# Performance work log

Measured on AMD Instinct MI355X. Metric: run time of the kernel, lower is better.

Reference implementation:

```python
import jax, jax.numpy as jnp
import numpy as np

ETA_MU = 0.01
ETA_VAR = 0.02
T, D = 32768, 1024


def setup_inputs() -> dict:
    key = jax.random.key(0)
    x = jax.random.normal(key, (T, D), dtype=jnp.float32)
    return {"x": x}


def reference(x):
    # x: [T, D]. Initial state: column mean and (unbiased) std, as in torch.mean/torch.std.
    mu0 = jnp.mean(x, axis=0)
    var0 = jnp.std(x, axis=0, ddof=1)  # torch.std default is unbiased; stored into 'var' slot

    eta_mu = jnp.float32(ETA_MU)
    eta_var = jnp.float32(ETA_VAR)

    def step(carry, xt):
        mu, var = carry
        mu = mu + eta_mu * (xt - mu)                      # in-place mu update (uses new mu below)
        var = var * (1 - eta_var) + eta_var * (xt - mu) ** 2
        norm = (xt - mu) / jnp.sqrt(var)
        return (mu, var), (norm, mu, var)

    _, (norm_x, mus, vars_) = jax.lax.scan(step, (mu0, var0), x)
    additional_info = jnp.concatenate([mus, vars_], axis=-1)  # [T, 2D]
    return norm_x, additional_info
```

## Files before the change

kernel.cpp:

```cpp
#include <hip/hip_runtime.h>
#include <math.h>


#define T_DIM 32768
#define D_DIM 1024
#define CHUNK 128
#define CLEN  (T_DIM / CHUNK)
#define ETA_MU_F 0.01f
#define ETA_VAR_F 0.02f

__global__ __launch_bounds__(256) void k_chunk_summary(
    const float* __restrict__ x, float* __restrict__ ws) {
    const int g = blockIdx.x * 256 + threadIdx.x;
    const int d = g & (D_DIM - 1);
    const int c = g >> 10;
    const float a = 1.0f - ETA_MU_F;
    const float b = 1.0f - ETA_VAR_F;

    float s = 0.0f, s2 = 0.0f;
    float m = 0.0f;
    float q0 = 0.0f, q1 = 0.0f, q2 = 0.0f;
    float p = 1.0f;

    const float* xp = x + (size_t)c * CLEN * D_DIM + d;
#pragma unroll 4
    for (int k = 0; k < CLEN; ++k) {
        float xv = xp[(size_t)k * D_DIM];
        s  += xv;
        s2 += xv * xv;
        m = m + ETA_MU_F * (xv - m);
        p *= a;
        float dv = xv - m;
        q0 = b * q0 + ETA_VAR_F * dv * dv;
        q1 = b * q1 - 2.0f * ETA_VAR_F * dv * p;
        q2 = b * q2 + ETA_VAR_F * p * p;
    }
    const int n = CHUNK * D_DIM;
    ws[0 * n + g] = s;
    ws[1 * n + g] = s2;
    ws[2 * n + g] = m;
    ws[3 * n + g] = q0;
    ws[4 * n + g] = q1;
    ws[5 * n + g] = q2;
}

__global__ __launch_bounds__(256) void k_scan(
    float* __restrict__ ws, float a_pow, float b_pow) {
    const int d = blockIdx.x * 256 + threadIdx.x;
    const int n = CHUNK * D_DIM;
    const float* sum  = ws + 0 * n;
    const float* sum2 = ws + 1 * n;
    const float* bmu  = ws + 2 * n;
    const float* q0   = ws + 3 * n;
    const float* q1   = ws + 4 * n;
    const float* q2   = ws + 5 * n;
    float* mu_in  = ws + 6 * n;
    float* var_in = ws + 7 * n;

    float s = 0.0f, s2 = 0.0f;
#pragma unroll 8
    for (int c = 0; c < CHUNK; ++c) {
        s  += sum[c * D_DIM + d];
        s2 += sum2[c * D_DIM + d];
    }
    float mu0 = s / (float)T_DIM;
    float v0  = (s2 - (float)T_DIM * mu0 * mu0) / (float)(T_DIM - 1);
    float std0 = sqrtf(fmaxf(v0, 0.0f));

    float mu = mu0;
    float var = std0;
#pragma unroll 4
    for (int c = 0; c < CHUNK; ++c) {
        int idx = c * D_DIM + d;
        mu_in[idx]  = mu;
        var_in[idx] = var;
        float mu_next = a_pow * mu + bmu[idx];
        var = b_pow * var + q0[idx] + mu * (q1[idx] + q2[idx] * mu);
        mu = mu_next;
    }
}

__global__ __launch_bounds__(256) void k_replay(
    const float* __restrict__ x, const float* __restrict__ ws,
    float* __restrict__ out) {
    const int g = blockIdx.x * 256 + threadIdx.x;
    const int d = g & (D_DIM - 1);
    const int c = g >> 10;
    const int n = CHUNK * D_DIM;

    float mu  = ws[6 * n + g];
    float var = ws[7 * n + g];

    const size_t t0 = (size_t)c * CLEN;
    const float* xp = x + t0 * D_DIM + d;
    float* norm_out = out + t0 * D_DIM + d;
    float* info = out + (size_t)T_DIM * D_DIM + t0 * (2 * D_DIM) + d;

#pragma unroll 4
    for (int k = 0; k < CLEN; ++k) {
        float xv = xp[(size_t)k * D_DIM];
        mu = mu + ETA_MU_F * (xv - mu);
        float diff = xv - mu;
        var = (1.0f - ETA_VAR_F) * var + ETA_VAR_F * diff * diff;
        norm_out[(size_t)k * D_DIM] = diff / sqrtf(var);
        info[(size_t)k * (2 * D_DIM)]         = mu;
        info[(size_t)k * (2 * D_DIM) + D_DIM] = var;
    }
}

extern "C" void kernel_launch(void* const* d_in, const int* in_sizes, int n_in,
                              void* d_out, int out_size, void* d_ws, size_t ws_size,
                              hipStream_t stream) {
    const float* x = (const float*)d_in[0];
    float* out = (float*)d_out;
    float* ws = (float*)d_ws;

    float a_pow = (float)pow(1.0 - 0.01, (double)CLEN);
    float b_pow = (float)pow(1.0 - 0.02, (double)CLEN);

    const int n = CHUNK * D_DIM;
    hipLaunchKernelGGL(k_chunk_summary, dim3(n / 256), dim3(256), 0, stream, x, ws);
    hipLaunchKernelGGL(k_scan, dim3(D_DIM / 256), dim3(256), 0, stream, ws, a_pow, b_pow);
    hipLaunchKernelGGL(k_replay, dim3(n / 256), dim3(256), 0, stream, x, ws, out);
}
```

Before: 577.7 us.

## Increase chunk count, vectorize float4 passes, fold q2 to host constant, nontemporal stores

Raises the number of time chunks from 128 to 512, which shortens each thread's serial recurrence and gives more parallelism, at the cost of a longer sequential scan over chunks. Chunk-summary and replay kernels now process four columns per thread with float4 loads and stores. The replay writes its outputs with nontemporal stores. The per-chunk q2 term, which depends only on constants, is precomputed on the host as a scalar, removing one workspace array and its loads. The scan kernel uses 64-thread blocks so more blocks spread across CUs, though its serial loop over 512 chunks is now longer.

```diff
diff --git a/kernel.cpp b/kernel.cpp
--- a/kernel.cpp
+++ b/kernel.cpp
@@ -4,58 +4,59 @@
 
 #define T_DIM 32768
 #define D_DIM 1024
-#define CHUNK 128
+#define CHUNK 512
 #define CLEN  (T_DIM / CHUNK)
 #define ETA_MU_F 0.01f
 #define ETA_VAR_F 0.02f
 
+typedef float vf4 __attribute__((ext_vector_type(4)));
+
 __global__ __launch_bounds__(256) void k_chunk_summary(
     const float* __restrict__ x, float* __restrict__ ws) {
-    const int g = blockIdx.x * 256 + threadIdx.x;
-    const int d = g & (D_DIM - 1);
-    const int c = g >> 10;
+    const int c = blockIdx.x;
+    const int j = threadIdx.x;
+    const int n = CHUNK * D_DIM;
     const float a = 1.0f - ETA_MU_F;
     const float b = 1.0f - ETA_VAR_F;
 
-    float s = 0.0f, s2 = 0.0f;
-    float m = 0.0f;
-    float q0 = 0.0f, q1 = 0.0f, q2 = 0.0f;
+    vf4 s  = {0.0f, 0.0f, 0.0f, 0.0f};
+    vf4 s2 = {0.0f, 0.0f, 0.0f, 0.0f};
+    vf4 m  = {0.0f, 0.0f, 0.0f, 0.0f};
+    vf4 q0 = {0.0f, 0.0f, 0.0f, 0.0f};
+    vf4 q1 = {0.0f, 0.0f, 0.0f, 0.0f};
     float p = 1.0f;
 
-    const float* xp = x + (size_t)c * CLEN * D_DIM + d;
-#pragma unroll 4
+    const vf4* xp = (const vf4*)(x + (size_t)c * CLEN * D_DIM) + j;
+#pragma unroll 8
     for (int k = 0; k < CLEN; ++k) {
-        float xv = xp[(size_t)k * D_DIM];
+        vf4 xv = xp[(size_t)k * (D_DIM / 4)];
+        p *= a;
         s  += xv;
         s2 += xv * xv;
-        m = m + ETA_MU_F * (xv - m);
-        p *= a;
-        float dv = xv - m;
-        q0 = b * q0 + ETA_VAR_F * dv * dv;
-        q1 = b * q1 - 2.0f * ETA_VAR_F * dv * p;
-        q2 = b * q2 + ETA_VAR_F * p * p;
+        m  += ETA_MU_F * (xv - m);
+        vf4 dv = xv - m;
+        q0 = b * q0 + ETA_VAR_F * (dv * dv);
+        q1 = b * q1 - (2.0f * ETA_VAR_F * p) * dv;
     }
-    const int n = CHUNK * D_DIM;
-    ws[0 * n + g] = s;
-    ws[1 * n + g] = s2;
-    ws[2 * n + g] = m;
-    ws[3 * n + g] = q0;
-    ws[4 * n + g] = q1;
-    ws[5 * n + g] = q2;
+    const int base = c * D_DIM + 4 * j;
+    *(vf4*)(ws + 0 * n + base) = s;
+    *(vf4*)(ws + 1 * n + base) = s2;
+    *(vf4*)(ws + 2 * n + base) = m;
+    *(vf4*)(ws + 3 * n + base) = q0;
+    *(vf4*)(ws + 4 * n + base) = q1;
 }
 
-__global__ __launch_bounds__(256) void k_scan(
-    float* __restrict__ ws, float a_pow, float b_pow) {
-    const int d = blockIdx.x * 256 + threadIdx.x;
+__global__ __launch_bounds__(64) void k_scan(
+    float* __restrict__ ws, float a_pow, float b_pow, float q2c) {
+    const int d = blockIdx.x * 64 + threadIdx.x;
     const int n = CHUNK * D_DIM;
     const float* sum  = ws + 0 * n;
     const float* sum2 = ws + 1 * n;
     const float* bmu  = ws + 2 * n;
     const float* q0   = ws + 3 * n;
     const float* q1   = ws + 4 * n;
-    const float* q2   = ws + 5 * n;
-    float* mu_in  = ws + 6 * n;
-    float* var_in = ws + 7 * n;
+    float* mu_in  = ws + 5 * n;
+    float* var_in = ws + 6 * n;
 
     float s = 0.0f, s2 = 0.0f;
 #pragma unroll 8
@@ -75,7 +76,7 @@
         mu_in[idx]  = mu;
         var_in[idx] = var;
         float mu_next = a_pow * mu + bmu[idx];
-        var = b_pow * var + q0[idx] + mu * (q1[idx] + q2[idx] * mu);
+        var = b_pow * var + q0[idx] + mu * (q1[idx] + q2c * mu);
         mu = mu_next;
     }
 }
@@ -83,28 +84,35 @@
 __global__ __launch_bounds__(256) void k_replay(
     const float* __restrict__ x, const float* __restrict__ ws,
     float* __restrict__ out) {
-    const int g = blockIdx.x * 256 + threadIdx.x;
-    const int d = g & (D_DIM - 1);
-    const int c = g >> 10;
+    const int c = blockIdx.x;
+    const int j = threadIdx.x;
     const int n = CHUNK * D_DIM;
+    const int base = c * D_DIM + 4 * j;
 
-    float mu  = ws[6 * n + g];
-    float var = ws[7 * n + g];
+    vf4 mu  = *(const vf4*)(ws + 5 * n + base);
+    vf4 var = *(const vf4*)(ws + 6 * n + base);
 
     const size_t t0 = (size_t)c * CLEN;
-    const float* xp = x + t0 * D_DIM + d;
-    float* norm_out = out + t0 * D_DIM + d;
-    float* info = out + (size_t)T_DIM * D_DIM + t0 * (2 * D_DIM) + d;
+    const vf4* xp = (const vf4*)(x + t0 * D_DIM) + j;
+    vf4* norm_out = (vf4*)(out + t0 * D_DIM) + j;
+    float* info_base = out + (size_t)T_DIM * D_DIM + t0 * (2 * D_DIM);
+    vf4* mu_out  = (vf4*)(info_base) + j;
+    vf4* var_out = (vf4*)(info_base + D_DIM) + j;
 
 #pragma unroll 4
     for (int k = 0; k < CLEN; ++k) {
-        float xv = xp[(size_t)k * D_DIM];
-        mu = mu + ETA_MU_F * (xv - mu);
-        float diff = xv - mu;
-        var = (1.0f - ETA_VAR_F) * var + ETA_VAR_F * diff * diff;
-        norm_out[(size_t)k * D_DIM] = diff / sqrtf(var);
-        info[(size_t)k * (2 * D_DIM)]         = mu;
-        info[(size_t)k * (2 * D_DIM) + D_DIM] = var;
+        vf4 xv = xp[(size_t)k * (D_DIM / 4)];
+        mu += ETA_MU_F * (xv - mu);
+        vf4 diff = xv - mu;
+        var = (1.0f - ETA_VAR_F) * var + ETA_VAR_F * (diff * diff);
+        vf4 nrm;
+        nrm.x = diff.x / sqrtf(var.x);
+        nrm.y = diff.y / sqrtf(var.y);
+        nrm.z = diff.z / sqrtf(var.z);
+        nrm.w = diff.w / sqrtf(var.w);
+        __builtin_nontemporal_store(nrm, norm_out + (size_t)k * (D_DIM / 4));
+        __builtin_nontemporal_store(mu,  mu_out  + (size_t)k * (2 * D_DIM / 4));
+        __builtin_nontemporal_store(var, var_out + (size_t)k * (2 * D_DIM / 4));
     }
 }
 
@@ -118,8 +126,14 @@
     float a_pow = (float)pow(1.0 - 0.01, (double)CLEN);
     float b_pow = (float)pow(1.0 - 0.02, (double)CLEN);
 
-    const int n = CHUNK * D_DIM;
-    hipLaunchKernelGGL(k_chunk_summary, dim3(n / 256), dim3(256), 0, stream, x, ws);
-    hipLaunchKernelGGL(k_scan, dim3(D_DIM / 256), dim3(256), 0, stream, ws, a_pow, b_pow);
-    hipLaunchKernelGGL(k_replay, dim3(n / 256), dim3(256), 0, stream, x, ws, out);
+    double q2d = 0.0;
+    for (int k = 0; k < CLEN; ++k) {
+        double pk = pow(0.99, (double)(k + 1));
+        q2d = 0.98 * q2d + 0.02 * pk * pk;
+    }
+    float q2c = (float)q2d;
+
+    hipLaunchKernelGGL(k_chunk_summary, dim3(CHUNK), dim3(256), 0, stream, x, ws);
+    hipLaunchKernelGGL(k_scan, dim3(D_DIM / 64), dim3(64), 0, stream, ws, a_pow, b_pow, q2c);
+    hipLaunchKernelGGL(k_replay, dim3(CHUNK), dim3(256), 0, stream, x, ws, out);
 }
```

New measurement: 653.4 us. 1.13x slower.
